# Optimization experiments

Measured on AMD Instinct MI355X. Metric: run time of the kernel, lower is better.

The kernel has to match this reference:

```python
import jax, jax.numpy as jnp
import numpy as np

IMG_FEAT = 2048
HIDDEN = 1024
K_TIMES = 3
GLIMPSE = 8
BA_HIDDEN = K_TIMES * HIDDEN  # 3072


def setup_inputs() -> dict:
    key = jax.random.key(0)
    ks = jax.random.split(key, 9)
    b, n_v, n_q = 64, 128, 32
    v = jax.random.normal(ks[0], (b, n_v, IMG_FEAT), dtype=jnp.float32)
    q = jax.random.normal(ks[1], (b, n_q, HIDDEN), dtype=jnp.float32)
    # weight-normed Linear params (weight_norm with dim=None -> scalar g)
    v_w = jax.random.normal(ks[2], (BA_HIDDEN, IMG_FEAT), dtype=jnp.float32) * 0.02
    v_g = jnp.asarray(jnp.linalg.norm(v_w), dtype=jnp.float32)
    v_b = jnp.zeros((BA_HIDDEN,), dtype=jnp.float32)
    q_w = jax.random.normal(ks[3], (BA_HIDDEN, HIDDEN), dtype=jnp.float32) * 0.02
    q_g = jnp.asarray(jnp.linalg.norm(q_w), dtype=jnp.float32)
    q_b = jnp.zeros((BA_HIDDEN,), dtype=jnp.float32)
    h_mat = jax.random.normal(ks[4], (1, GLIMPSE, 1, BA_HIDDEN), dtype=jnp.float32)
    h_bias = jax.random.normal(ks[5], (1, GLIMPSE, 1, 1), dtype=jnp.float32)
    return {"v": v, "q": q, "v_w": v_w, "v_g": v_g, "v_b": v_b,
            "q_w": q_w, "q_g": q_g, "q_b": q_b,
            "h_mat": h_mat, "h_bias": h_bias}


def _wn_linear_relu(x, w, g, b):
    # weight_norm(dim=None): w_eff = g * w / ||w||_F (scalar g)
    w_eff = (g / jnp.linalg.norm(w)) * w
    return jax.nn.relu(jnp.einsum('bnd,kd->bnk', x, w_eff) + b)


def reference(v, q, v_w, v_g, v_b, q_w, q_g, q_b, h_mat, h_bias):
    # dropout layers are identity in eval mode
    v_ = _wn_linear_relu(v, v_w, v_g, v_b)  # [b, n_v, K]
    q_ = _wn_linear_relu(q, q_w, q_g, q_b)  # [b, n_q, K]
    # einsum('xhyk,bvk,bqk->bhvq') with h_mat [1,g,1,K]
    hm = h_mat[0, :, 0, :]  # [g, K]
    logits = jnp.einsum('hk,bvk,bqk->bhvq', hm, v_, q_) + h_bias
    return logits
```

## Files before the change

### kernel.cpp

```cpp
#include <hip/hip_runtime.h>

typedef __attribute__((ext_vector_type(8))) __bf16 bf16x8;
typedef __attribute__((ext_vector_type(4))) float f32x4;
typedef const __attribute__((address_space(1))) unsigned int gas_u32;
typedef __attribute__((address_space(3))) unsigned int las_u32;

__device__ __forceinline__ unsigned short f2bf(float f) {
  unsigned u = __builtin_bit_cast(unsigned, f);
  u = (u + 0x7FFFu + ((u >> 16) & 1u)) >> 16;
  return (unsigned short)u;
}
__device__ __forceinline__ float bf2f(unsigned short h) {
  return __builtin_bit_cast(float, (unsigned)h << 16);
}

__global__ __launch_bounds__(256) void k_prep(
    const float* __restrict__ v, const float* __restrict__ q,
    const float* __restrict__ vw, const float* __restrict__ qw,
    unsigned short* __restrict__ v_bf, unsigned short* __restrict__ q_bf,
    unsigned short* __restrict__ vw_bf, unsigned short* __restrict__ qw_bf,
    float* __restrict__ ss) {
  __shared__ float red[4];
  int bid = blockIdx.x, tid = threadIdx.x;
  const float* in;
  unsigned short* out;
  float* ssout = nullptr;
  int n8, b0, nb;
  if (bid < 768) {
    in = v; out = v_bf; n8 = 2097152; b0 = bid; nb = 768;
  } else if (bid < 864) {
    in = q; out = q_bf; n8 = 262144; b0 = bid - 768; nb = 96;
  } else if (bid < 1344) {
    in = vw; out = vw_bf; n8 = 786432; b0 = bid - 864; nb = 480; ssout = ss + 0;
  } else {
    in = qw; out = qw_bf; n8 = 393216; b0 = bid - 1344; nb = 192; ssout = ss + 1;
  }
  float s = 0.f;
  for (int i = b0 * 256 + tid; i < n8; i += nb * 256) {
    float4 a = ((const float4*)in)[2 * i];
    float4 b = ((const float4*)in)[2 * i + 1];
    if (ssout) {
      s += a.x * a.x + a.y * a.y + a.z * a.z + a.w * a.w;
      s += b.x * b.x + b.y * b.y + b.z * b.z + b.w * b.w;
    }
    uint4 o;
    o.x = f2bf(a.x) | ((unsigned)f2bf(a.y) << 16);
    o.y = f2bf(a.z) | ((unsigned)f2bf(a.w) << 16);
    o.z = f2bf(b.x) | ((unsigned)f2bf(b.y) << 16);
    o.w = f2bf(b.z) | ((unsigned)f2bf(b.w) << 16);
    ((uint4*)out)[i] = o;
  }
  if (ssout) {
    for (int off = 32; off; off >>= 1) s += __shfl_down(s, off);
    if ((tid & 63) == 0) red[tid >> 6] = s;
    __syncthreads();
    if (tid == 0) atomicAdd(ssout, red[0] + red[1] + red[2] + red[3]);
  }
}

__global__ __launch_bounds__(256, 2) void k_gemm_wn(
    const unsigned short* __restrict__ A, const unsigned short* __restrict__ B,
    const float* __restrict__ bias, const float* __restrict__ gptr,
    const float* __restrict__ ssptr, unsigned short* __restrict__ C,
    int M, int N, int K, int nbn) {
  __shared__ __align__(16) unsigned short lA[2 * 128 * 64];
  __shared__ __align__(16) unsigned short lB[2 * 192 * 64];
  const int tid = threadIdx.x;
  const int wid = tid >> 6, lane = tid & 63;
  const int l15 = lane & 15, l4 = lane >> 4;
  const int wm = wid >> 1, wn = wid & 1;
  const int rr8 = tid >> 3;
  const int scol8 = (((tid & 7)) ^ (rr8 & 7)) << 3;

  int nwg = gridDim.x;
  int wg = (blockIdx.x & 7) * (nwg >> 3) + (blockIdx.x >> 3);
  int bm = wg / nbn, bn = wg % nbn;

  const unsigned short* Ab = A + (size_t)bm * 128 * K;
  const unsigned short* Bb = B + (size_t)bn * 192 * K;
  const int nt = K >> 6;

#define SB() __builtin_amdgcn_sched_barrier(0);

#define STAGE_A(U, TS)                                                             \
  {                                                                                \
    int ts_ = (TS) < nt ? (TS) : nt - 1;                                           \
    _Pragma("unroll") for (int j = 0; j < 2; ++j) {                                \
      __builtin_amdgcn_global_load_lds(                                            \
          (gas_u32*)(Ab + (size_t)((U)*64 + j * 32 + rr8) * K + ts_ * 64 + scol8), \
          (las_u32*)(lA + ((TS)&1) * 8192 + (U)*4096 + j * 2048 + tid * 8), 16, 0, \
          0);                                                                      \
    }                                                                              \
  }

#define STAGE_B(U, TS)                                                             \
  {                                                                                \
    int ts_ = (TS) < nt ? (TS) : nt - 1;                                           \
    _Pragma("unroll") for (int j = 0; j < 2; ++j) {                                \
      __builtin_amdgcn_global_load_lds(                                            \
          (gas_u32*)(Bb + (size_t)((U)*64 + j * 32 + rr8) * K + ts_ * 64 + scol8), \
          (las_u32*)(lB + ((TS)&1) * 12288 + (U)*4096 + j * 2048 + tid * 8), 16,   \
          0, 0);                                                                   \
    }                                                                              \
  }

#define LDSA(DST, MQ, TP)                                                          \
  _Pragma("unroll") for (int i2 = 0; i2 < 2; ++i2) {                               \
    int rl = wm * 64 + ((MQ)*2 + i2) * 16 + l15;                                   \
    const unsigned short* ap = lA + (TP)*8192 + rl * 64;                           \
    int s8 = rl & 7;                                                               \
    DST[i2][0] = *(const bf16x8*)(ap + ((l4 ^ s8) << 3));                          \
    DST[i2][1] = *(const bf16x8*)(ap + (((4 | l4) ^ s8) << 3));                    \
  }

#define LDSB(DST, NQ, TP)                                                          \
  _Pragma("unroll") for (int j3 = 0; j3 < 3; ++j3) {                               \
    int rl = wn * 96 + ((NQ)*3 + j3) * 16 + l15;                                   \
    const unsigned short* bp = lB + (TP)*12288 + rl * 64;                          \
    int s8 = rl & 7;                                                               \
    DST[j3][0] = *(const bf16x8*)(bp + ((l4 ^ s8) << 3));                          \
    DST[j3][1] = *(const bf16x8*)(bp + (((4 | l4) ^ s8) << 3));                    \
  }

#define MFMA12(MQ, NQ, AF, BF)                                                     \
  _Pragma("unroll") for (int ks = 0; ks < 2; ++ks)                                 \
  _Pragma("unroll") for (int i2 = 0; i2 < 2; ++i2)                                 \
  _Pragma("unroll") for (int j3 = 0; j3 < 3; ++j3)                                 \
    acc[(MQ)*2 + i2][(NQ)*3 + j3] = __builtin_amdgcn_mfma_f32_16x16x32_bf16(       \
        AF[i2][ks], BF[j3][ks], acc[(MQ)*2 + i2][(NQ)*3 + j3], 0, 0, 0);

  f32x4 acc[4][6] = {};
  bf16x8 a0_[2][2], a1_[2][2], b0_[3][2], b1_[3][2];

  STAGE_A(0, 0) STAGE_A(1, 0) STAGE_B(0, 0) STAGE_B(1, 0) STAGE_B(2, 0)
  STAGE_A(0, 1) STAGE_A(1, 1)
  asm volatile("s_waitcnt vmcnt(4)" ::: "memory");
  SB()
  __builtin_amdgcn_s_barrier();
  LDSA(a0_, 0, 0)
  STAGE_B(0, 1) STAGE_B(1, 1)
  LDSB(b0_, 0, 0)

  for (int t = 0; t < nt; ++t) {
    const int cp = t & 1, np = (t + 1) & 1;
    LDSB(b1_, 1, cp)
    STAGE_B(2, t + 1)
    __builtin_amdgcn_s_setprio(1);
    MFMA12(0, 0, a0_, b0_)
    __builtin_amdgcn_s_setprio(0);
    LDSA(a1_, 1, cp)
    __builtin_amdgcn_s_setprio(1);
    MFMA12(0, 1, a0_, b1_)
    __builtin_amdgcn_s_setprio(0);
    asm volatile("s_waitcnt lgkmcnt(0)" ::: "memory");
    asm volatile("s_waitcnt vmcnt(6)" ::: "memory");
    SB()
    __builtin_amdgcn_s_barrier();
    LDSA(a0_, 0, np)
    STAGE_A(0, t + 2) STAGE_A(1, t + 2)
    __builtin_amdgcn_s_setprio(1);
    MFMA12(1, 0, a1_, b0_)
    __builtin_amdgcn_s_setprio(0);
    asm volatile("s_waitcnt vmcnt(4)" ::: "memory");
    SB()
    __builtin_amdgcn_s_barrier();
    LDSB(b0_, 0, np)
    STAGE_B(0, t + 2) STAGE_B(1, t + 2)
    __builtin_amdgcn_s_setprio(1);
    MFMA12(1, 1, a1_, b1_)
    __builtin_amdgcn_s_setprio(0);
  }

  asm volatile("s_waitcnt vmcnt(0)" ::: "memory");

  float s = gptr[0] / sqrtf(ssptr[0]);
#pragma unroll
  for (int nj = 0; nj < 6; ++nj) {
    int gcol = bn * 192 + wn * 96 + nj * 16 + l15;
    float bv = bias[gcol];
#pragma unroll
    for (int mi = 0; mi < 4; ++mi) {
#pragma unroll
      for (int r = 0; r < 4; ++r) {
        int grow = bm * 128 + wm * 64 + mi * 16 + l4 * 4 + r;
        float v = fmaxf(acc[mi][nj][r] * s + bv, 0.f);
        C[(size_t)grow * N + gcol] = f2bf(v);
      }
    }
  }
#undef STAGE_A
#undef STAGE_B
#undef LDSA
#undef LDSB
#undef MFMA12
#undef SB
}

__global__ __launch_bounds__(256, 2) void k_gemm_bt(
    const unsigned short* __restrict__ A, const unsigned short* __restrict__ B,
    const float* __restrict__ bias, const float* __restrict__ gptr,
    const float* __restrict__ ssptr, unsigned short* __restrict__ C,
    int M, int N, int K, int nbm) {
  __shared__ __align__(16) unsigned short lA[128 * 64];
  __shared__ __align__(16) unsigned short lB[128 * 64];
  int tid = threadIdx.x;
  int wid = tid >> 6, lane = tid & 63;
  int l15 = lane & 15, l4 = lane >> 4;
  int w0 = wid >> 1, w1 = wid & 1;

  int nwg = gridDim.x;
  int wg = (blockIdx.x & 7) * (nwg >> 3) + (blockIdx.x >> 3);
  int bm = wg % nbm, bn = wg / nbm;

  const unsigned short* Ab = A + (size_t)bm * 128 * K;
  const unsigned short* Bb = B + (size_t)bn * 128 * K;

  f32x4 acc[4][4] = {};

  for (int k0 = 0; k0 < K; k0 += 64) {
    __syncthreads();
#pragma unroll
    for (int i = 0; i < 4; ++i) {
      int ebase = (i * 4 + wid) << 9;
      int eoff = ebase + lane * 8;
      int row = eoff >> 6, col = eoff & 63;
      __builtin_amdgcn_global_load_lds(
          (gas_u32*)(Ab + (size_t)row * K + k0 + col),
          (las_u32*)(lA + ebase), 16, 0, 0);
      __builtin_amdgcn_global_load_lds(
          (gas_u32*)(Bb + (size_t)row * K + k0 + col),
          (las_u32*)(lB + ebase), 16, 0, 0);
    }
    __syncthreads();
#pragma unroll
    for (int ks = 0; ks < 2; ++ks) {
      bf16x8 af[4], bfr[4];
#pragma unroll
      for (int mi = 0; mi < 4; ++mi)
        af[mi] = *(const bf16x8*)(lA + ((w0 * 64 + mi * 16 + l15) * 64 + ks * 32 + l4 * 8));
#pragma unroll
      for (int nj = 0; nj < 4; ++nj)
        bfr[nj] = *(const bf16x8*)(lB + ((w1 * 64 + nj * 16 + l15) * 64 + ks * 32 + l4 * 8));
#pragma unroll
      for (int mi = 0; mi < 4; ++mi)
#pragma unroll
        for (int nj = 0; nj < 4; ++nj)
          acc[mi][nj] =
              __builtin_amdgcn_mfma_f32_16x16x32_bf16(af[mi], bfr[nj], acc[mi][nj], 0, 0, 0);
    }
  }

  float s = gptr[0] / sqrtf(ssptr[0]);
#pragma unroll
  for (int mi = 0; mi < 4; ++mi)
#pragma unroll
    for (int nj = 0; nj < 4; ++nj) {
      int col = bn * 128 + w1 * 64 + nj * 16 + l15;
      float bv = bias[col];
#pragma unroll
      for (int r = 0; r < 4; ++r) {
        int row = bm * 128 + w0 * 64 + mi * 16 + l4 * 4 + r;
        float v = fmaxf(acc[mi][nj][r] * s + bv, 0.f);
        C[(size_t)row * N + col] = f2bf(v);
      }
    }
}

__global__ __launch_bounds__(256, 2) void k_glimpse5(
    const unsigned short* __restrict__ Vh, const unsigned short* __restrict__ Qh,
    const float* __restrict__ hmat, const float* __restrict__ hbias,
    float* __restrict__ out) {
  __shared__ __align__(16) unsigned short lV[3][64 * 64];
  __shared__ __align__(16) unsigned short lQ[2][4][32 * 64];
  int tid = threadIdx.x;
  int wid = tid >> 6, lane = tid & 63;
  int l15 = lane & 15, l4 = lane >> 4;

  int id = blockIdx.x;
  int b = id & 63, hv = id >> 6;
  int h4 = hv & 1, vh = hv >> 1;

  const unsigned short* Vb = Vh + (size_t)b * 128 * 3072 + (size_t)vh * 64 * 3072;
  const unsigned short* Qb = Qh + (size_t)b * 32 * 3072;
  const float* hr0 = hmat + (h4 * 4 + 0) * 3072;
  const float* hr1 = hmat + (h4 * 4 + 1) * 3072;
  const float* hr2 = hmat + (h4 * 4 + 2) * 3072;
  const float* hr3 = hmat + (h4 * 4 + 3) * 3072;

  f32x4 acc[4][2] = {};
  const int rr8 = tid >> 3;
  const int ch8 = tid & 7;
  const int scol8 = (ch8 ^ (rr8 & 7)) << 3;
  const int qwoff = rr8 * 64 + scol8;
  const int qc = ch8 * 8;
  const int NT = 48;

#define VSTAGE(T, SLOT)                                                          \
  {                                                                              \
    int tc = (T) < NT ? (T) : NT - 1;                                            \
    _Pragma("unroll") for (int j = 0; j < 2; ++j) {                              \
      __builtin_amdgcn_global_load_lds(                                          \
          (gas_u32*)(Vb + (size_t)(j * 32 + rr8) * 3072 + tc * 64 + scol8),      \
          (las_u32*)(&lV[SLOT][0] + j * 2048 + tid * 8), 16, 0, 0);              \
    }                                                                            \
  }

#define QLOAD(T, RQ, H)                                                          \
  {                                                                              \
    int tc = (T) < NT ? (T) : NT - 1;                                            \
    RQ = *(const uint4*)(Qb + (size_t)rr8 * 3072 + tc * 64 + qc);                \
    H[0] = ((const float4*)(hr0 + tc * 64 + qc))[0];                             \
    H[1] = ((const float4*)(hr0 + tc * 64 + qc))[1];                             \
    H[2] = ((const float4*)(hr1 + tc * 64 + qc))[0];                             \
    H[3] = ((const float4*)(hr1 + tc * 64 + qc))[1];                             \
    H[4] = ((const float4*)(hr2 + tc * 64 + qc))[0];                             \
    H[5] = ((const float4*)(hr2 + tc * 64 + qc))[1];                             \
    H[6] = ((const float4*)(hr3 + tc * 64 + qc))[0];                             \
    H[7] = ((const float4*)(hr3 + tc * 64 + qc))[1];                             \
  }

#define QWRITE(CB, RQ, H)                                                        \
  {                                                                              \
    float e0 = bf2f((unsigned short)(RQ.x & 0xffff));                            \
    float e1 = bf2f((unsigned short)(RQ.x >> 16));                               \
    float e2 = bf2f((unsigned short)(RQ.y & 0xffff));                            \
    float e3 = bf2f((unsigned short)(RQ.y >> 16));                               \
    float e4 = bf2f((unsigned short)(RQ.z & 0xffff));                            \
    float e5 = bf2f((unsigned short)(RQ.z >> 16));                               \
    float e6 = bf2f((unsigned short)(RQ.w & 0xffff));                            \
    float e7 = bf2f((unsigned short)(RQ.w >> 16));                               \
    _Pragma("unroll") for (int hh = 0; hh < 4; ++hh) {                           \
      uint4 o;                                                                   \
      o.x = f2bf(e0 * H[hh * 2].x) | ((unsigned)f2bf(e1 * H[hh * 2].y) << 16);   \
      o.y = f2bf(e2 * H[hh * 2].z) | ((unsigned)f2bf(e3 * H[hh * 2].w) << 16);   \
      o.z = f2bf(e4 * H[hh * 2 + 1].x) |                                         \
            ((unsigned)f2bf(e5 * H[hh * 2 + 1].y) << 16);                        \
      o.w = f2bf(e6 * H[hh * 2 + 1].z) |                                         \
            ((unsigned)f2bf(e7 * H[hh * 2 + 1].w) << 16);                        \
      *(uint4*)(&lQ[CB][hh][0] + qwoff) = o;                                     \
    }                                                                            \
  }

#define GMFMA(SLOT, CB)                                                          \
  {                                                                              \
    int rlv = wid * 16 + l15;                                                    \
    int s8v = rlv & 7;                                                           \
    bf16x8 af[2];                                                                \
    af[0] = *(const bf16x8*)(&lV[SLOT][0] + rlv * 64 + ((l4 ^ s8v) << 3));       \
    af[1] = *(const bf16x8*)(&lV[SLOT][0] + rlv * 64 + (((4 | l4) ^ s8v) << 3)); \
    _Pragma("unroll") for (int hh = 0; hh < 4; ++hh) {                           \
      _Pragma("unroll") for (int nj = 0; nj < 2; ++nj) {                         \
        int rlq = nj * 16 + l15;                                                 \
        int s8q = rlq & 7;                                                       \
        bf16x8 bq0 = *(const bf16x8*)(&lQ[CB][hh][0] + rlq * 64 +                \
                                      ((l4 ^ s8q) << 3));                        \
        bf16x8 bq1 = *(const bf16x8*)(&lQ[CB][hh][0] + rlq * 64 +                \
                                      (((4 | l4) ^ s8q) << 3));                  \
        acc[hh][nj] =                                                            \
            __builtin_amdgcn_mfma_f32_16x16x32_bf16(af[0], bq0, acc[hh][nj], 0, 0, 0); \
        acc[hh][nj] =                                                            \
            __builtin_amdgcn_mfma_f32_16x16x32_bf16(af[1], bq1, acc[hh][nj], 0, 0, 0); \
      }                                                                          \
    }                                                                            \
  }

#define GBODY(T, CQ, CH, NQ, NH)                                                 \
  {                                                                              \
    QLOAD((T) + 2, NQ, NH)                                                       \
    asm volatile("s_waitcnt vmcnt(11)" ::: "memory");                            \
    asm volatile("s_waitcnt lgkmcnt(0)" ::: "memory");                           \
    __builtin_amdgcn_sched_barrier(0);                                           \
    __builtin_amdgcn_s_barrier();                                                \
    VSTAGE((T) + 2, ((T) + 2) % 3)                                               \
    QWRITE(((T) + 1) & 1, CQ, CH)                                                \
    GMFMA((T) % 3, (T) & 1)                                                      \
  }

  uint4 aq, bq_;
  float4 ah[8], bh[8];

  QLOAD(0, aq, ah)
  QLOAD(1, bq_, bh)
  VSTAGE(0, 0)
  VSTAGE(1, 1)
  asm volatile("s_waitcnt vmcnt(13)" ::: "memory");
  __builtin_amdgcn_sched_barrier(0);
  QWRITE(0, aq, ah)

  for (int t = 0; t < NT; t += 2) {
    GBODY(t, bq_, bh, aq, ah)
    GBODY(t + 1, aq, ah, bq_, bh)
  }
  asm volatile("s_waitcnt vmcnt(0) lgkmcnt(0)" ::: "memory");

#pragma unroll
  for (int hh = 0; hh < 4; ++hh) {
    int h = h4 * 4 + hh;
    float hb = hbias[h];
    float* ob = out + (size_t)(b * 8 + h) * 128 * 32;
#pragma unroll
    for (int nj = 0; nj < 2; ++nj)
#pragma unroll
      for (int r = 0; r < 4; ++r) {
        int row = vh * 64 + wid * 16 + l4 * 4 + r;
        int col = nj * 16 + l15;
        ob[row * 32 + col] = acc[hh][nj][r] + hb;
      }
  }
#undef VSTAGE
#undef QLOAD
#undef QWRITE
#undef GMFMA
#undef GBODY
}

extern "C" void kernel_launch(void* const* d_in, const int* in_sizes, int n_in,
                              void* d_out, int out_size, void* d_ws, size_t ws_size,
                              hipStream_t stream) {
  const float* v = (const float*)d_in[0];
  const float* q = (const float*)d_in[1];
  const float* v_w = (const float*)d_in[2];
  const float* v_g = (const float*)d_in[3];
  const float* v_b = (const float*)d_in[4];
  const float* q_w = (const float*)d_in[5];
  const float* q_g = (const float*)d_in[6];
  const float* q_b = (const float*)d_in[7];
  const float* hmat = (const float*)d_in[8];
  const float* hbias = (const float*)d_in[9];
  float* out = (float*)d_out;

  const size_t n_v = 16777216;
  const size_t n_vw = 6291456;
  const size_t n_q = 2097152;
  const size_t n_qw = 3145728;
  const size_t n_vh = 25165824;
  const size_t n_qh = 6291456;

  char* ws = (char*)d_ws;
  float* ss = (float*)ws;
  size_t off = 256;
  unsigned short* v_bf = (unsigned short*)(ws + off);  off += n_v * 2;
  unsigned short* vw_bf = (unsigned short*)(ws + off); off += n_vw * 2;
  unsigned short* q_bf = (unsigned short*)(ws + off);  off += n_q * 2;
  unsigned short* qw_bf = (unsigned short*)(ws + off); off += n_qw * 2;
  unsigned short* v_h = (unsigned short*)(ws + off);   off += n_vh * 2;
  unsigned short* q_h = (unsigned short*)(ws + off);   off += n_qh * 2;

  (void)hipMemsetAsync(ss, 0, 8, stream);
  k_prep<<<1536, 256, 0, stream>>>(v, q, v_w, q_w, v_bf, q_bf, vw_bf, qw_bf, ss);

  k_gemm_wn<<<1024, 256, 0, stream>>>(v_bf, vw_bf, v_b, v_g, ss + 0, v_h,
                                      8192, 3072, 2048, 16);
  k_gemm_bt<<<384, 256, 0, stream>>>(q_bf, qw_bf, q_b, q_g, ss + 1, q_h,
                                     2048, 3072, 1024, 16);

  k_glimpse5<<<256, 256, 0, stream>>>(v_h, q_h, hmat, hbias, out);
}
```

Baseline: 219.3 us.

## Merge V and Q projection GEMMs into one launch using the pipelined kernel

Replaces the separate V-projection and Q-projection GEMM launches with a single combined kernel. Blocks below 1024 handle V and the remaining 256 handle Q, so the Q GEMM now uses the pipelined double-buffered 128x192 path instead of the simple 128x128 kernel. The change also precomputes per-row staging pointers and unrolls the K loop by two to make buffer indices compile-time constants. Separately, the glimpse kernel's block-to-batch mapping is reordered so that neighbouring blocks share the same batch's V and Q rows. The cost is more branching at block start and an assumption that nt is even.

```diff
diff --git a/kernel.cpp b/kernel.cpp
--- a/kernel.cpp
+++ b/kernel.cpp
@@ -58,11 +58,13 @@
   }
 }
 
-__global__ __launch_bounds__(256, 2) void k_gemm_wn(
-    const unsigned short* __restrict__ A, const unsigned short* __restrict__ B,
-    const float* __restrict__ bias, const float* __restrict__ gptr,
-    const float* __restrict__ ssptr, unsigned short* __restrict__ C,
-    int M, int N, int K, int nbn) {
+__global__ __launch_bounds__(256, 2) void k_gemm_cmb(
+    const unsigned short* __restrict__ A1, const unsigned short* __restrict__ B1,
+    const float* __restrict__ bias1, const float* __restrict__ g1,
+    const float* __restrict__ ss1, unsigned short* __restrict__ C1,
+    const unsigned short* __restrict__ A2, const unsigned short* __restrict__ B2,
+    const float* __restrict__ bias2, const float* __restrict__ g2,
+    const float* __restrict__ ss2, unsigned short* __restrict__ C2) {
   __shared__ __align__(16) unsigned short lA[2 * 128 * 64];
   __shared__ __align__(16) unsigned short lB[2 * 192 * 64];
   const int tid = threadIdx.x;
@@ -70,38 +72,64 @@
   const int l15 = lane & 15, l4 = lane >> 4;
   const int wm = wid >> 1, wn = wid & 1;
   const int rr8 = tid >> 3;
-  const int scol8 = (((tid & 7)) ^ (rr8 & 7)) << 3;
-
-  int nwg = gridDim.x;
-  int wg = (blockIdx.x & 7) * (nwg >> 3) + (blockIdx.x >> 3);
-  int bm = wg / nbn, bn = wg % nbn;
+  const int scol8 = ((tid & 7) ^ (rr8 & 7)) << 3;
+
+  const unsigned short* A;
+  const unsigned short* B;
+  const float* bias;
+  const float* gptr;
+  const float* ssptr;
+  unsigned short* C;
+  int K, nt, wg;
+  if (blockIdx.x < 1024) {
+    int bid = blockIdx.x;
+    wg = (bid & 7) * 128 + (bid >> 3);
+    A = A1; B = B1; bias = bias1; gptr = g1; ssptr = ss1; C = C1;
+    K = 2048; nt = 32;
+  } else {
+    int bid = blockIdx.x - 1024;
+    wg = (bid & 7) * 32 + (bid >> 3);
+    A = A2; B = B2; bias = bias2; gptr = g2; ssptr = ss2; C = C2;
+    K = 1024; nt = 16;
+  }
+  const int bm = wg >> 4, bn = wg & 15;
 
   const unsigned short* Ab = A + (size_t)bm * 128 * K;
   const unsigned short* Bb = B + (size_t)bn * 192 * K;
-  const int nt = K >> 6;
+
+  const unsigned short* sA00 = Ab + (size_t)(rr8) * K + scol8;
+  const unsigned short* sA01 = Ab + (size_t)(32 + rr8) * K + scol8;
+  const unsigned short* sA10 = Ab + (size_t)(64 + rr8) * K + scol8;
+  const unsigned short* sA11 = Ab + (size_t)(96 + rr8) * K + scol8;
+  const unsigned short* sB00 = Bb + (size_t)(rr8) * K + scol8;
+  const unsigned short* sB01 = Bb + (size_t)(32 + rr8) * K + scol8;
+  const unsigned short* sB10 = Bb + (size_t)(64 + rr8) * K + scol8;
+  const unsigned short* sB11 = Bb + (size_t)(96 + rr8) * K + scol8;
+  const unsigned short* sB20 = Bb + (size_t)(128 + rr8) * K + scol8;
+  const unsigned short* sB21 = Bb + (size_t)(160 + rr8) * K + scol8;
 
 #define SB() __builtin_amdgcn_sched_barrier(0);
 
-#define STAGE_A(U, TS)                                                             \
+#define STAGE_A(U, TS, BUFI)                                                       \
   {                                                                                \
     int ts_ = (TS) < nt ? (TS) : nt - 1;                                           \
-    _Pragma("unroll") for (int j = 0; j < 2; ++j) {                                \
-      __builtin_amdgcn_global_load_lds(                                            \
-          (gas_u32*)(Ab + (size_t)((U)*64 + j * 32 + rr8) * K + ts_ * 64 + scol8), \
-          (las_u32*)(lA + ((TS)&1) * 8192 + (U)*4096 + j * 2048 + tid * 8), 16, 0, \
-          0);                                                                      \
-    }                                                                              \
-  }
-
-#define STAGE_B(U, TS)                                                             \
+    __builtin_amdgcn_global_load_lds(                                              \
+        (gas_u32*)(sA##U##0 + (size_t)ts_ * 64),                                   \
+        (las_u32*)(lA + (BUFI)*8192 + (U)*4096 + tid * 8), 16, 0, 0);              \
+    __builtin_amdgcn_global_load_lds(                                              \
+        (gas_u32*)(sA##U##1 + (size_t)ts_ * 64),                                   \
+        (las_u32*)(lA + (BUFI)*8192 + (U)*4096 + 2048 + tid * 8), 16, 0, 0);       \
+  }
+
+#define STAGE_B(U, TS, BUFI)                                                       \
   {                                                                                \
     int ts_ = (TS) < nt ? (TS) : nt - 1;                                           \
-    _Pragma("unroll") for (int j = 0; j < 2; ++j) {                                \
-      __builtin_amdgcn_global_load_lds(                                            \
-          (gas_u32*)(Bb + (size_t)((U)*64 + j * 32 + rr8) * K + ts_ * 64 + scol8), \
-          (las_u32*)(lB + ((TS)&1) * 12288 + (U)*4096 + j * 2048 + tid * 8), 16,   \
-          0, 0);                                                                   \
-    }                                                                              \
+    __builtin_amdgcn_global_load_lds(                                              \
+        (gas_u32*)(sB##U##0 + (size_t)ts_ * 64),                                   \
+        (las_u32*)(lB + (BUFI)*12288 + (U)*4096 + tid * 8), 16, 0, 0);             \
+    __builtin_amdgcn_global_load_lds(                                              \
+        (gas_u32*)(sB##U##1 + (size_t)ts_ * 64),                                   \
+        (las_u32*)(lB + (BUFI)*12288 + (U)*4096 + 2048 + tid * 8), 16, 0, 0);      \
   }
 
 #define LDSA(DST, MQ, TP)                                                          \
@@ -129,50 +157,54 @@
     acc[(MQ)*2 + i2][(NQ)*3 + j3] = __builtin_amdgcn_mfma_f32_16x16x32_bf16(       \
         AF[i2][ks], BF[j3][ks], acc[(MQ)*2 + i2][(NQ)*3 + j3], 0, 0, 0);
 
+#define TILE_BODY(T, CP, NP)                                                       \
+  LDSB(b1_, 1, CP)                                                                 \
+  STAGE_B(2, (T) + 1, NP)                                                          \
+  __builtin_amdgcn_s_setprio(1);                                                   \
+  MFMA12(0, 0, a0_, b0_)                                                           \
+  __builtin_amdgcn_s_setprio(0);                                                   \
+  LDSA(a1_, 1, CP)                                                                 \
+  __builtin_amdgcn_s_setprio(1);                                                   \
+  MFMA12(0, 1, a0_, b1_)                                                           \
+  __builtin_amdgcn_s_setprio(0);                                                   \
+  asm volatile("s_waitcnt lgkmcnt(0)" ::: "memory");                               \
+  asm volatile("s_waitcnt vmcnt(6)" ::: "memory");                                 \
+  SB()                                                                             \
+  __builtin_amdgcn_s_barrier();                                                    \
+  LDSA(a0_, 0, NP)                                                                 \
+  STAGE_A(0, (T) + 2, CP) STAGE_A(1, (T) + 2, CP)                                  \
+  __builtin_amdgcn_s_setprio(1);                                                   \
+  MFMA12(1, 0, a1_, b0_)                                                           \
+  __builtin_amdgcn_s_setprio(0);                                                   \
+  asm volatile("s_waitcnt vmcnt(4)" ::: "memory");                                 \
+  SB()                                                                             \
+  __builtin_amdgcn_s_barrier();                                                    \
+  LDSB(b0_, 0, NP)                                                                 \
+  STAGE_B(0, (T) + 2, CP) STAGE_B(1, (T) + 2, CP)                                  \
+  __builtin_amdgcn_s_setprio(1);                                                   \
+  MFMA12(1, 1, a1_, b1_)                                                           \
+  __builtin_amdgcn_s_setprio(0);
+
   f32x4 acc[4][6] = {};
   bf16x8 a0_[2][2], a1_[2][2], b0_[3][2], b1_[3][2];
 
-  STAGE_A(0, 0) STAGE_A(1, 0) STAGE_B(0, 0) STAGE_B(1, 0) STAGE_B(2, 0)
-  STAGE_A(0, 1) STAGE_A(1, 1)
+  STAGE_A(0, 0, 0) STAGE_A(1, 0, 0) STAGE_B(0, 0, 0) STAGE_B(1, 0, 0) STAGE_B(2, 0, 0)
+  STAGE_A(0, 1, 1) STAGE_A(1, 1, 1)
   asm volatile("s_waitcnt vmcnt(4)" ::: "memory");
   SB()
   __builtin_amdgcn_s_barrier();
   LDSA(a0_, 0, 0)
-  STAGE_B(0, 1) STAGE_B(1, 1)
+  STAGE_B(0, 1, 1) STAGE_B(1, 1, 1)
   LDSB(b0_, 0, 0)
 
-  for (int t = 0; t < nt; ++t) {
-    const int cp = t & 1, np = (t + 1) & 1;
-    LDSB(b1_, 1, cp)
-    STAGE_B(2, t + 1)
-    __builtin_amdgcn_s_setprio(1);
-    MFMA12(0, 0, a0_, b0_)
-    __builtin_amdgcn_s_setprio(0);
-    LDSA(a1_, 1, cp)
-    __builtin_amdgcn_s_setprio(1);
-    MFMA12(0, 1, a0_, b1_)
-    __builtin_amdgcn_s_setprio(0);
-    asm volatile("s_waitcnt lgkmcnt(0)" ::: "memory");
-    asm volatile("s_waitcnt vmcnt(6)" ::: "memory");
-    SB()
-    __builtin_amdgcn_s_barrier();
-    LDSA(a0_, 0, np)
-    STAGE_A(0, t + 2) STAGE_A(1, t + 2)
-    __builtin_amdgcn_s_setprio(1);
-    MFMA12(1, 0, a1_, b0_)
-    __builtin_amdgcn_s_setprio(0);
-    asm volatile("s_waitcnt vmcnt(4)" ::: "memory");
-    SB()
-    __builtin_amdgcn_s_barrier();
-    LDSB(b0_, 0, np)
-    STAGE_B(0, t + 2) STAGE_B(1, t + 2)
-    __builtin_amdgcn_s_setprio(1);
-    MFMA12(1, 1, a1_, b1_)
-    __builtin_amdgcn_s_setprio(0);
+  for (int t = 0; t < nt; t += 2) {
+    TILE_BODY(t, 0, 1)
+    TILE_BODY(t + 1, 1, 0)
   }
 
   asm volatile("s_waitcnt vmcnt(0)" ::: "memory");
 
+  const int N = 3072;
   float s = gptr[0] / sqrtf(ssptr[0]);
 #pragma unroll
   for (int nj = 0; nj < 6; ++nj) {
@@ -193,77 +225,8 @@
 #undef LDSA
 #undef LDSB
 #undef MFMA12
+#undef TILE_BODY
 #undef SB
-}
-
-__global__ __launch_bounds__(256, 2) void k_gemm_bt(
-    const unsigned short* __restrict__ A, const unsigned short* __restrict__ B,
-    const float* __restrict__ bias, const float* __restrict__ gptr,
-    const float* __restrict__ ssptr, unsigned short* __restrict__ C,
-    int M, int N, int K, int nbm) {
-  __shared__ __align__(16) unsigned short lA[128 * 64];
-  __shared__ __align__(16) unsigned short lB[128 * 64];
-  int tid = threadIdx.x;
-  int wid = tid >> 6, lane = tid & 63;
-  int l15 = lane & 15, l4 = lane >> 4;
-  int w0 = wid >> 1, w1 = wid & 1;
-
-  int nwg = gridDim.x;
-  int wg = (blockIdx.x & 7) * (nwg >> 3) + (blockIdx.x >> 3);
-  int bm = wg % nbm, bn = wg / nbm;
-
-  const unsigned short* Ab = A + (size_t)bm * 128 * K;
-  const unsigned short* Bb = B + (size_t)bn * 128 * K;
-
-  f32x4 acc[4][4] = {};
-
-  for (int k0 = 0; k0 < K; k0 += 64) {
-    __syncthreads();
-#pragma unroll
-    for (int i = 0; i < 4; ++i) {
-      int ebase = (i * 4 + wid) << 9;
-      int eoff = ebase + lane * 8;
-      int row = eoff >> 6, col = eoff & 63;
-      __builtin_amdgcn_global_load_lds(
-          (gas_u32*)(Ab + (size_t)row * K + k0 + col),
-          (las_u32*)(lA + ebase), 16, 0, 0);
-      __builtin_amdgcn_global_load_lds(
-          (gas_u32*)(Bb + (size_t)row * K + k0 + col),
-          (las_u32*)(lB + ebase), 16, 0, 0);
-    }
-    __syncthreads();
-#pragma unroll
-    for (int ks = 0; ks < 2; ++ks) {
-      bf16x8 af[4], bfr[4];
-#pragma unroll
-      for (int mi = 0; mi < 4; ++mi)
-        af[mi] = *(const bf16x8*)(lA + ((w0 * 64 + mi * 16 + l15) * 64 + ks * 32 + l4 * 8));
-#pragma unroll
-      for (int nj = 0; nj < 4; ++nj)
-        bfr[nj] = *(const bf16x8*)(lB + ((w1 * 64 + nj * 16 + l15) * 64 + ks * 32 + l4 * 8));
-#pragma unroll
-      for (int mi = 0; mi < 4; ++mi)
-#pragma unroll
-        for (int nj = 0; nj < 4; ++nj)
-          acc[mi][nj] =
-              __builtin_amdgcn_mfma_f32_16x16x32_bf16(af[mi], bfr[nj], acc[mi][nj], 0, 0, 0);
-    }
-  }
-
-  float s = gptr[0] / sqrtf(ssptr[0]);
-#pragma unroll
-  for (int mi = 0; mi < 4; ++mi)
-#pragma unroll
-    for (int nj = 0; nj < 4; ++nj) {
-      int col = bn * 128 + w1 * 64 + nj * 16 + l15;
-      float bv = bias[col];
-#pragma unroll
-      for (int r = 0; r < 4; ++r) {
-        int row = bm * 128 + w0 * 64 + mi * 16 + l4 * 4 + r;
-        float v = fmaxf(acc[mi][nj][r] * s + bv, 0.f);
-        C[(size_t)row * N + col] = f2bf(v);
-      }
-    }
 }
 
 __global__ __launch_bounds__(256, 2) void k_glimpse5(
@@ -277,7 +240,7 @@
   int l15 = lane & 15, l4 = lane >> 4;
 
   int id = blockIdx.x;
-  int b = id & 63, hv = id >> 6;
+  int b = id >> 2, hv = id & 3;
   int h4 = hv & 1, vh = hv >> 1;
 
   const unsigned short* Vb = Vh + (size_t)b * 128 * 3072 + (size_t)vh * 64 * 3072;
@@ -449,10 +412,8 @@
   (void)hipMemsetAsync(ss, 0, 8, stream);
   k_prep<<<1536, 256, 0, stream>>>(v, q, v_w, q_w, v_bf, q_bf, vw_bf, qw_bf, ss);
 
-  k_gemm_wn<<<1024, 256, 0, stream>>>(v_bf, vw_bf, v_b, v_g, ss + 0, v_h,
-                                      8192, 3072, 2048, 16);
-  k_gemm_bt<<<384, 256, 0, stream>>>(q_bf, qw_bf, q_b, q_g, ss + 1, q_h,
-                                     2048, 3072, 1024, 16);
+  k_gemm_cmb<<<1280, 256, 0, stream>>>(v_bf, vw_bf, v_b, v_g, ss + 0, v_h,
+                                       q_bf, qw_bf, q_b, q_g, ss + 1, q_h);
 
   k_glimpse5<<<256, 256, 0, stream>>>(v_h, q_h, hmat, hbias, out);
 }
```

After: 208.0 us. -5.2%, faster.
